# Kernel tuning notes

Hardware: AMD Instinct MI355X
Metric: run time of the kernel (lower is better)

## Reference

```python
import jax, jax.numpy as jnp
import numpy as np

B, S, T = 32, 128, 128
V, E, H = 32000, 256, 256
PAD_IDX = 0


def setup_inputs() -> dict:
    key = jax.random.key(0)
    ks = jax.random.split(key, 12)
    p = lambda k, shape: jax.random.normal(k, shape, dtype=jnp.float32) * 0.05
    src = jax.random.randint(ks[0], (B, S), 0, V)
    tgt = jax.random.randint(ks[1], (B, T), 0, V)
    enc_emb = p(ks[2], (V, E)).at[PAD_IDX].set(0.0)
    dec_emb = p(ks[3], (V, E)).at[PAD_IDX].set(0.0)
    return {
        'src': src,
        'tgt': tgt,
        'enc_emb': enc_emb,
        'enc_Wih': p(ks[4], (4 * H, E)),
        'enc_Whh': p(ks[5], (4 * H, H)),
        'enc_b': p(ks[6], (4 * H,)),
        'dec_emb': dec_emb,
        'dec_Wih': p(ks[7], (4 * H, E)),
        'dec_Whh': p(ks[8], (4 * H, H)),
        'dec_b': p(ks[9], (4 * H,)),
        'fc_W': p(ks[10], (V, H)),
        'fc_b': p(ks[11], (V,)),
    }


def lstm_scan(x_seq, h0, c0, Wih, Whh, b):
    # x_seq: [L, B, E] -> hs: [L, B, H]; PyTorch gate order i, f, g, o
    def step(carry, x):
        h, c = carry
        gates = x @ Wih.T + h @ Whh.T + b  # [B, 4H]
        i, f, g, o = jnp.split(gates, 4, axis=-1)
        c = jax.nn.sigmoid(f) * c + jax.nn.sigmoid(i) * jnp.tanh(g)
        h = jax.nn.sigmoid(o) * jnp.tanh(c)
        return (h, c), h
    (h, c), hs = jax.lax.scan(step, (h0, c0), x_seq)
    return hs, (h, c)


def reference(src, tgt, enc_emb, enc_Wih, enc_Whh, enc_b,
              dec_emb, dec_Wih, dec_Whh, dec_b, fc_W, fc_b):
    bs, tgt_len = tgt.shape
    # Encoder: embed + single-layer LSTM, keep final (h, c)
    x = jnp.swapaxes(enc_emb[src], 0, 1)            # [S, B, E]
    h0 = jnp.zeros((bs, enc_Whh.shape[1]), x.dtype)
    _, (h, c) = lstm_scan(x, h0, h0, enc_Wih, enc_Whh, enc_b)
    # Decoder with full teacher forcing (tf_ratio=1.0):
    # input at step t is tgt[:, t-1]; outputs[:, 0] stays zero.
    dec_in = jnp.swapaxes(dec_emb[tgt[:, :-1]], 0, 1)  # [T-1, B, E]
    hs, _ = lstm_scan(dec_in, h, c, dec_Wih, dec_Whh, dec_b)  # [T-1, B, H]
    logits = jnp.einsum('tbh,vh->btv', hs, fc_W) + fc_b        # [B, T-1, V]
    outputs = jnp.zeros((bs, tgt_len, fc_W.shape[0]), logits.dtype)
    return outputs.at[:, 1:].set(logits)
```

## Files before the change

kernel.cpp:

```cpp
#include <hip/hip_runtime.h>


typedef __attribute__((ext_vector_type(8))) short bf16x8;
typedef __attribute__((ext_vector_type(4))) float f32x4;
typedef __attribute__((ext_vector_type(8))) unsigned short u16x8;
typedef __attribute__((ext_vector_type(4))) unsigned int u32x4;
typedef __attribute__((ext_vector_type(8))) _Float16 f16x8;
typedef __attribute__((ext_vector_type(2))) _Float16 h2;

#define WS_XG_E   0u
#define WS_XG_D   16777216u
#define WS_FCW    33423360u
#define WS_HS     49807360u
#define WS_WTE    51904512u
#define WS_WTD    52428800u

#define KC_REG 48
#define KC_LDS 16

__device__ __forceinline__ unsigned short f2bf(float f) {
  unsigned u = __float_as_uint(f);
  u += 0x7FFFu + ((u >> 16) & 1u);
  return (unsigned short)(u >> 16);
}

__device__ __forceinline__ float sigf(float x) {
  float e = __expf(-x);
  return __builtin_amdgcn_rcpf(1.f + e);
}
__device__ __forceinline__ float tanh_fast(float x) {
  float e = __expf(-2.f * x);
  return fmaf(2.f, __builtin_amdgcn_rcpf(1.f + e), -1.f);
}

#if __has_builtin(__builtin_amdgcn_fdot2)
#define FDOT2(a, w, h) a = __builtin_amdgcn_fdot2(w, h, a, false)
#else
#define FDOT2(a, w, h) a = fmaf((float)w[0], (float)h[0], fmaf((float)w[1], (float)h[1], a))
#endif

__device__ __forceinline__ void dot8(const u16x8 w, const u32x4 hbits,
                                     float& a0, float& a1) {
  f16x8 wv = __builtin_bit_cast(f16x8, w);
  f16x8 hv = __builtin_bit_cast(f16x8, hbits);
  h2 w0 = {wv[0], wv[1]}, w1 = {wv[2], wv[3]};
  h2 w2 = {wv[4], wv[5]}, w3 = {wv[6], wv[7]};
  h2 h0 = {hv[0], hv[1]}, h1 = {hv[2], hv[3]};
  h2 hc = {hv[4], hv[5]}, h3 = {hv[6], hv[7]};
  FDOT2(a0, w0, h0);
  FDOT2(a1, w1, h1);
  FDOT2(a0, w2, hc);
  FDOT2(a1, w3, h3);
}

__global__ __launch_bounds__(256) void zero_col0(float* __restrict__ out) {
  int i = blockIdx.x * 256 + threadIdx.x;
  int b = i / 8000;
  int r = i - b * 8000;
  f32x4 z = {0.f, 0.f, 0.f, 0.f};
  __builtin_nontemporal_store(z, (f32x4*)out + b * 1024000 + r);
}

__global__ __launch_bounds__(256) void cvt_bf16(const float* __restrict__ in,
                                                unsigned short* __restrict__ o,
                                                int n4) {
  int i = blockIdx.x * 256 + threadIdx.x;
  if (i < n4) {
    float4 v = ((const float4*)in)[i];
    ushort4 u;
    u.x = f2bf(v.x); u.y = f2bf(v.y); u.z = f2bf(v.z); u.w = f2bf(v.w);
    *(ushort4*)(o + i * 4) = u;
  }
}

__global__ __launch_bounds__(256) void prep_whalf(const float* __restrict__ We,
                                                  const float* __restrict__ Wd,
                                                  unsigned short* __restrict__ Te,
                                                  unsigned short* __restrict__ Td) {
  int d = blockIdx.x * 256 + threadIdx.x;
  const float* W = blockIdx.y ? Wd : We;
  unsigned short* T = blockIdx.y ? Td : Te;
  int e = d & 7;
  int tmp = d >> 3;
  int tidb = tmp & 511;
  int j = tmp >> 9;
  int gg = j >> 4, kk = j & 15;
  int wv = tidb >> 6, ln = tidb & 63;
  int qq = ln >> 5, dm = wv * 32 + (ln & 31);
  _Float16 v = (_Float16)W[(gg * 256 + dm) * 256 + qq * 128 + kk * 8 + e];
  T[d] = __builtin_bit_cast(unsigned short, v);
}

__global__ __launch_bounds__(256) void xg_gemm(
    const int* __restrict__ tok, const float* __restrict__ emb,
    const float* __restrict__ Wih, const float* __restrict__ bias,
    float* __restrict__ xg, const int Mrows) {
  __shared__ unsigned short As[128][264];
  __shared__ unsigned short Bs[128][264];
  const int tid = threadIdx.x;
  const int nb = blockIdx.x, rb = blockIdx.y;
  {
    int lr = tid >> 1, half = tid & 1;
    int cb = half * 128;
    int row = rb * 128 + lr;
    int rowc = row < Mrows ? row : (Mrows - 1);
    int tt = rowc >> 5, bb = rowc & 31;
    int tk = tok[bb * 128 + tt];
    const float4* sa = (const float4*)(emb + tk * 256 + cb);
    const float4* sb = (const float4*)(Wih + (nb * 128 + lr) * 256 + cb);
#pragma unroll
    for (int i = 0; i < 32; ++i) {
      float4 v = sa[i];
      ushort4 u;
      u.x = f2bf(v.x); u.y = f2bf(v.y); u.z = f2bf(v.z); u.w = f2bf(v.w);
      *(ushort4*)&As[lr][cb + i * 4] = u;
      float4 v2 = sb[i];
      ushort4 u2;
      u2.x = f2bf(v2.x); u2.y = f2bf(v2.y); u2.z = f2bf(v2.z); u2.w = f2bf(v2.w);
      *(ushort4*)&Bs[lr][cb + i * 4] = u2;
    }
  }
  __syncthreads();
  const int lane = tid & 63, w = tid >> 6;
  const int wr = w >> 1, wc = w & 1;
  const int fr = lane & 15, kg = lane >> 4;
  f32x4 acc[4][4];
  const f32x4 zero = {0.f, 0.f, 0.f, 0.f};
#pragma unroll
  for (int mi = 0; mi < 4; ++mi)
#pragma unroll
    for (int ni = 0; ni < 4; ++ni) acc[mi][ni] = zero;
#pragma unroll
  for (int ks = 0; ks < 8; ++ks) {
    const int kb = ks * 32 + kg * 8;
    bf16x8 a[4], b[4];
#pragma unroll
    for (int mi = 0; mi < 4; ++mi)
      a[mi] = *(const bf16x8*)&As[wr * 64 + mi * 16 + fr][kb];
#pragma unroll
    for (int ni = 0; ni < 4; ++ni)
      b[ni] = *(const bf16x8*)&Bs[wc * 64 + ni * 16 + fr][kb];
#pragma unroll
    for (int mi = 0; mi < 4; ++mi)
#pragma unroll
      for (int ni = 0; ni < 4; ++ni)
        acc[mi][ni] = __builtin_amdgcn_mfma_f32_16x16x32_bf16(a[mi], b[ni], acc[mi][ni], 0, 0, 0);
  }
#pragma unroll
  for (int ni = 0; ni < 4; ++ni) {
    const int colg = nb * 128 + wc * 64 + ni * 16 + fr;
    const float bv = bias[colg];
#pragma unroll
    for (int mi = 0; mi < 4; ++mi) {
#pragma unroll
      for (int r = 0; r < 4; ++r) {
        int rowg = rb * 128 + wr * 64 + mi * 16 + kg * 4 + r;
        if (rowg < Mrows) xg[rowg * 1024 + colg] = acc[mi][ni][r] + bv;
      }
    }
  }
}

__global__ __launch_bounds__(512, 2) void lstm_batch(
    const unsigned short* __restrict__ WTe, const unsigned short* __restrict__ WTd,
    const float* __restrict__ xgE, const float* __restrict__ xgD,
    unsigned short* __restrict__ hs) {
  __shared__ __align__(16) unsigned short hh[2][256];
  __shared__ __align__(16) unsigned short wl[KC_LDS * 4096];
  const int tid = threadIdx.x;
  const int b = blockIdx.x;
  const int l = tid & 63, w = tid >> 6;
  const int q = l >> 5;
  const int dim = w * 32 + (l & 31);
  float c = 0.f;
  int cur = 0;
  if (tid < 256) hh[0][tid] = 0;

  for (int phase = 0; phase < 2; ++phase) {
    const unsigned short* WT = phase ? WTd : WTe;
    const float* xg = phase ? xgD : xgE;
    const int steps = phase ? 127 : 128;
    const u16x8* wsrc = (const u16x8*)WT + tid;
    u16x8 wr[KC_REG];
#pragma unroll
    for (int j = 0; j < KC_REG; ++j) wr[j] = wsrc[j * 512];
    __syncthreads();
    {
      u16x8* ld = (u16x8*)wl + tid;
#pragma unroll
      for (int j = 0; j < KC_LDS; ++j) ld[j * 512] = wsrc[(KC_REG + j) * 512];
    }
    __syncthreads();

    for (int t = 0; t < steps; ++t) {
      const float* xr = xg + (t * 32 + b) * 1024 + dim;
      float x0 = xr[0], x1 = xr[256], x2 = xr[512], x3 = xr[768];
      const u32x4* hq = (const u32x4*)&hh[cur][q * 128];
      const u16x8* wlp = (const u16x8*)wl + tid;
      float ai0 = 0.f, ai1 = 0.f, af0 = 0.f, af1 = 0.f;
      float ag0 = 0.f, ag1 = 0.f, ao0 = 0.f, ao1 = 0.f;
#pragma unroll
      for (int kk = 0; kk < 16; ++kk) {
        u32x4 hv = hq[kk];
        dot8(wr[kk],        hv, ai0, ai1);
        dot8(wr[16 + kk],   hv, af0, af1);
        dot8(wr[32 + kk],   hv, ag0, ag1);
        dot8(wlp[kk * 512], hv, ao0, ao1);
      }
      float gi = ai0 + ai1, gf = af0 + af1;
      float gg = ag0 + ag1, go = ao0 + ao1;
      gi += __shfl_xor(gi, 32, 64);
      gf += __shfl_xor(gf, 32, 64);
      gg += __shfl_xor(gg, 32, 64);
      go += __shfl_xor(go, 32, 64);
      gi += x0; gf += x1; gg += x2; go += x3;
      c = sigf(gf) * c + sigf(gi) * tanh_fast(gg);
      float h = sigf(go) * tanh_fast(c);
      if (l < 32) {
        _Float16 hf = (_Float16)h;
        hh[cur ^ 1][dim] = __builtin_bit_cast(unsigned short, hf);
        if (phase) hs[(b * 128 + t) * 256 + dim] = f2bf(h);
      }
      __syncthreads();
      cur ^= 1;
    }
  }
}

__global__ __launch_bounds__(256) void fc_gemm(
    const unsigned short* __restrict__ hsb, const unsigned short* __restrict__ fwb,
    const float* __restrict__ fcb, float* __restrict__ out) {
  __shared__ __align__(16) char smem[69632];
  typedef unsigned short usrow[136];
  usrow* As = (usrow*)smem;
  usrow* Bs = (usrow*)(smem + 34816);
  const int tid = threadIdx.x;
  const int rb = blockIdx.x, nb = blockIdx.y;
  const int lane = tid & 63, w = tid >> 6;
  const int wr = w >> 1, wc = w & 1;
  const int fr = lane & 15, kg = lane >> 4;
  f32x4 acc[4][4];
  const f32x4 zero = {0.f, 0.f, 0.f, 0.f};
#pragma unroll
  for (int mi = 0; mi < 4; ++mi)
#pragma unroll
    for (int ni = 0; ni < 4; ++ni) acc[mi][ni] = zero;

  const int lr = tid >> 1, half = tid & 1;
#pragma unroll
  for (int p = 0; p < 2; ++p) {
    {
      const u16x8* s = (const u16x8*)(hsb + (rb * 128 + lr) * 256 + p * 128 + half * 64);
      const u16x8* s2 = (const u16x8*)(fwb + (nb * 128 + lr) * 256 + p * 128 + half * 64);
      u16x8* d = (u16x8*)&As[lr][half * 64];
      u16x8* d2 = (u16x8*)&Bs[lr][half * 64];
#pragma unroll
      for (int i = 0; i < 8; ++i) { d[i] = s[i]; d2[i] = s2[i]; }
    }
    __syncthreads();
#pragma unroll
    for (int ks = 0; ks < 4; ++ks) {
      const int kb = ks * 32 + kg * 8;
      bf16x8 a[4], b[4];
#pragma unroll
      for (int mi = 0; mi < 4; ++mi)
        a[mi] = *(const bf16x8*)&As[wr * 64 + mi * 16 + fr][kb];
#pragma unroll
      for (int ni = 0; ni < 4; ++ni)
        b[ni] = *(const bf16x8*)&Bs[wc * 64 + ni * 16 + fr][kb];
#pragma unroll
      for (int mi = 0; mi < 4; ++mi)
#pragma unroll
        for (int ni = 0; ni < 4; ++ni)
          acc[mi][ni] = __builtin_amdgcn_mfma_f32_16x16x32_bf16(a[mi], b[ni], acc[mi][ni], 0, 0, 0);
    }
    __syncthreads();
  }
  typedef float frow[132];
  frow* Ct = (frow*)smem;
#pragma unroll
  for (int ni = 0; ni < 4; ++ni) {
    const int cl = wc * 64 + ni * 16 + fr;
    const float bv = fcb[nb * 128 + cl];
#pragma unroll
    for (int mi = 0; mi < 4; ++mi) {
#pragma unroll
      for (int r = 0; r < 4; ++r)
        Ct[wr * 64 + mi * 16 + kg * 4 + r][cl] = acc[mi][ni][r] + bv;
    }
  }
  __syncthreads();
  const int rr = tid >> 5, cc = (tid & 31) * 4;
#pragma unroll
  for (int p = 0; p < 16; ++p) {
    int r = p * 8 + rr;
    if (r != 127) {
      float* dst = out + (size_t)(rb * 128 + r + 1) * 32000 + nb * 128 + cc;
      f32x4 v = *(const f32x4*)&Ct[r][cc];
      __builtin_nontemporal_store(v, (f32x4*)dst);
    }
  }
}

extern "C" void kernel_launch(void* const* d_in, const int* in_sizes, int n_in,
                              void* d_out, int out_size, void* d_ws, size_t ws_size,
                              hipStream_t stream) {
  const int* src = (const int*)d_in[0];
  const int* tgt = (const int*)d_in[1];
  const float* enc_emb = (const float*)d_in[2];
  const float* enc_Wih = (const float*)d_in[3];
  const float* enc_Whh = (const float*)d_in[4];
  const float* enc_b = (const float*)d_in[5];
  const float* dec_emb = (const float*)d_in[6];
  const float* dec_Wih = (const float*)d_in[7];
  const float* dec_Whh = (const float*)d_in[8];
  const float* dec_b = (const float*)d_in[9];
  const float* fc_W = (const float*)d_in[10];
  const float* fc_b = (const float*)d_in[11];
  float* out = (float*)d_out;
  char* ws = (char*)d_ws;

  float* xg_e = (float*)(ws + WS_XG_E);
  float* xg_d = (float*)(ws + WS_XG_D);
  unsigned short* fcw = (unsigned short*)(ws + WS_FCW);
  unsigned short* hs = (unsigned short*)(ws + WS_HS);
  unsigned short* wte = (unsigned short*)(ws + WS_WTE);
  unsigned short* wtd = (unsigned short*)(ws + WS_WTD);

  zero_col0<<<1000, 256, 0, stream>>>(out);
  cvt_bf16<<<8000, 256, 0, stream>>>(fc_W, fcw, 2048000);
  prep_whalf<<<dim3(1024, 2), 256, 0, stream>>>(enc_Whh, dec_Whh, wte, wtd);
  xg_gemm<<<dim3(8, 32), 256, 0, stream>>>(src, enc_emb, enc_Wih, enc_b, xg_e, 4096);
  xg_gemm<<<dim3(8, 32), 256, 0, stream>>>(tgt, dec_emb, dec_Wih, dec_b, xg_d, 4064);
  lstm_batch<<<32, 512, 0, stream>>>(wte, wtd, xg_e, xg_d, hs);
  fc_gemm<<<dim3(32, 250), 256, 0, stream>>>(hs, fcw, fc_b, out);
}
```

Baseline: 678.4 us.

## Halve fc_gemm LDS by reading A fragments from global and staging output in halves

The FC GEMM no longer stages the hidden-state tile in shared memory. Each wave now loads its A fragments straight from global memory, which is small and cache-resident. The output epilogue is split into two 64-row passes so the C staging buffer fits in the same 34 KB, and launch bounds request 4 blocks per CU. Together these cut LDS use in half to allow more resident blocks. The cost is uncoalesced global A loads in the inner loop and an extra barrier round in the epilogue.

```diff
diff --git a/kernel.cpp b/kernel.cpp
--- a/kernel.cpp
+++ b/kernel.cpp
@@ -227,13 +227,12 @@
   }
 }
 
-__global__ __launch_bounds__(256) void fc_gemm(
+__global__ __launch_bounds__(256, 4) void fc_gemm(
     const unsigned short* __restrict__ hsb, const unsigned short* __restrict__ fwb,
     const float* __restrict__ fcb, float* __restrict__ out) {
-  __shared__ __align__(16) char smem[69632];
+  __shared__ __align__(16) char smem[34816];
   typedef unsigned short usrow[136];
-  usrow* As = (usrow*)smem;
-  usrow* Bs = (usrow*)(smem + 34816);
+  usrow* Bs = (usrow*)smem;
   const int tid = threadIdx.x;
   const int rb = blockIdx.x, nb = blockIdx.y;
   const int lane = tid & 63, w = tid >> 6;
@@ -247,15 +246,14 @@
     for (int ni = 0; ni < 4; ++ni) acc[mi][ni] = zero;
 
   const int lr = tid >> 1, half = tid & 1;
+  const unsigned short* arow = hsb + (rb * 128 + wr * 64 + fr) * 256;
 #pragma unroll
   for (int p = 0; p < 2; ++p) {
     {
-      const u16x8* s = (const u16x8*)(hsb + (rb * 128 + lr) * 256 + p * 128 + half * 64);
       const u16x8* s2 = (const u16x8*)(fwb + (nb * 128 + lr) * 256 + p * 128 + half * 64);
-      u16x8* d = (u16x8*)&As[lr][half * 64];
       u16x8* d2 = (u16x8*)&Bs[lr][half * 64];
 #pragma unroll
-      for (int i = 0; i < 8; ++i) { d[i] = s[i]; d2[i] = s2[i]; }
+      for (int i = 0; i < 8; ++i) d2[i] = s2[i];
     }
     __syncthreads();
 #pragma unroll
@@ -264,7 +262,7 @@
       bf16x8 a[4], b[4];
 #pragma unroll
       for (int mi = 0; mi < 4; ++mi)
-        a[mi] = *(const bf16x8*)&As[wr * 64 + mi * 16 + fr][kb];
+        a[mi] = *(const bf16x8*)(arow + mi * 4096 + p * 128 + kb);
 #pragma unroll
       for (int ni = 0; ni < 4; ++ni)
         b[ni] = *(const bf16x8*)&Bs[wc * 64 + ni * 16 + fr][kb];
@@ -276,29 +274,35 @@
     }
     __syncthreads();
   }
+  float bvv[4];
+#pragma unroll
+  for (int ni = 0; ni < 4; ++ni) bvv[ni] = fcb[nb * 128 + wc * 64 + ni * 16 + fr];
   typedef float frow[132];
   frow* Ct = (frow*)smem;
-#pragma unroll
-  for (int ni = 0; ni < 4; ++ni) {
-    const int cl = wc * 64 + ni * 16 + fr;
-    const float bv = fcb[nb * 128 + cl];
-#pragma unroll
-    for (int mi = 0; mi < 4; ++mi) {
-#pragma unroll
-      for (int r = 0; r < 4; ++r)
-        Ct[wr * 64 + mi * 16 + kg * 4 + r][cl] = acc[mi][ni][r] + bv;
-    }
-  }
-  __syncthreads();
   const int rr = tid >> 5, cc = (tid & 31) * 4;
 #pragma unroll
-  for (int p = 0; p < 16; ++p) {
-    int r = p * 8 + rr;
-    if (r != 127) {
-      float* dst = out + (size_t)(rb * 128 + r + 1) * 32000 + nb * 128 + cc;
-      f32x4 v = *(const f32x4*)&Ct[r][cc];
-      __builtin_nontemporal_store(v, (f32x4*)dst);
-    }
+  for (int hh2 = 0; hh2 < 2; ++hh2) {
+    if (wr == hh2) {
+#pragma unroll
+      for (int ni = 0; ni < 4; ++ni)
+#pragma unroll
+        for (int mi = 0; mi < 4; ++mi)
+#pragma unroll
+          for (int r = 0; r < 4; ++r)
+            Ct[mi * 16 + kg * 4 + r][wc * 64 + ni * 16 + fr] = acc[mi][ni][r] + bvv[ni];
+    }
+    __syncthreads();
+#pragma unroll
+    for (int pp = 0; pp < 8; ++pp) {
+      int r = pp * 8 + rr;
+      int tg = hh2 * 64 + r;
+      if (tg != 127) {
+        float* dst = out + (size_t)(rb * 128 + tg + 1) * 32000 + nb * 128 + cc;
+        f32x4 v = *(const f32x4*)&Ct[r][cc];
+        __builtin_nontemporal_store(v, (f32x4*)dst);
+      }
+    }
+    __syncthreads();
   }
 }
 
```

Result: slower. 730.2 us (+7.6%).

## Fuse zero column write into FC GEMM and halve M tile for occupancy

Applied to the files above, without the earlier changes.

Removes the separate zero_col0 kernel and has the FC GEMM write the zero row for t=0 in place of the out-of-range last row. The GEMM M tile shrinks from 128 to 64 rows, which doubles the grid, cuts LDS per block so three blocks can fit per CU, and halves the accumulators per wave. The trade-off is that each weight tile is loaded from global memory twice as often.

```diff
diff --git a/kernel.cpp b/kernel.cpp
--- a/kernel.cpp
+++ b/kernel.cpp
@@ -51,14 +51,6 @@
   FDOT2(a1, w1, h1);
   FDOT2(a0, w2, hc);
   FDOT2(a1, w3, h3);
-}
-
-__global__ __launch_bounds__(256) void zero_col0(float* __restrict__ out) {
-  int i = blockIdx.x * 256 + threadIdx.x;
-  int b = i / 8000;
-  int r = i - b * 8000;
-  f32x4 z = {0.f, 0.f, 0.f, 0.f};
-  __builtin_nontemporal_store(z, (f32x4*)out + b * 1024000 + r);
 }
 
 __global__ __launch_bounds__(256) void cvt_bf16(const float* __restrict__ in,
@@ -227,49 +219,52 @@
   }
 }
 
-__global__ __launch_bounds__(256) void fc_gemm(
+__global__ __launch_bounds__(256, 3) void fc_gemm(
     const unsigned short* __restrict__ hsb, const unsigned short* __restrict__ fwb,
     const float* __restrict__ fcb, float* __restrict__ out) {
-  __shared__ __align__(16) char smem[69632];
+  __shared__ __align__(16) char smem[52224];
   typedef unsigned short usrow[136];
   usrow* As = (usrow*)smem;
-  usrow* Bs = (usrow*)(smem + 34816);
+  usrow* Bs = (usrow*)(smem + 17408);
   const int tid = threadIdx.x;
   const int rb = blockIdx.x, nb = blockIdx.y;
   const int lane = tid & 63, w = tid >> 6;
-  const int wr = w >> 1, wc = w & 1;
+  const int wm = w & 1, wn = w >> 1;
   const int fr = lane & 15, kg = lane >> 4;
-  f32x4 acc[4][4];
+  f32x4 acc[2][4];
   const f32x4 zero = {0.f, 0.f, 0.f, 0.f};
 #pragma unroll
-  for (int mi = 0; mi < 4; ++mi)
+  for (int mi = 0; mi < 2; ++mi)
 #pragma unroll
     for (int ni = 0; ni < 4; ++ni) acc[mi][ni] = zero;
 
-  const int lr = tid >> 1, half = tid & 1;
+  const int ar = tid >> 2, asg = tid & 3;
+  const int br = tid >> 1, bsg = tid & 1;
 #pragma unroll
   for (int p = 0; p < 2; ++p) {
     {
-      const u16x8* s = (const u16x8*)(hsb + (rb * 128 + lr) * 256 + p * 128 + half * 64);
-      const u16x8* s2 = (const u16x8*)(fwb + (nb * 128 + lr) * 256 + p * 128 + half * 64);
-      u16x8* d = (u16x8*)&As[lr][half * 64];
-      u16x8* d2 = (u16x8*)&Bs[lr][half * 64];
-#pragma unroll
-      for (int i = 0; i < 8; ++i) { d[i] = s[i]; d2[i] = s2[i]; }
+      const u16x8* s = (const u16x8*)(hsb + (rb * 64 + ar) * 256 + p * 128 + asg * 32);
+      u16x8* d = (u16x8*)&As[ar][asg * 32];
+#pragma unroll
+      for (int i = 0; i < 4; ++i) d[i] = s[i];
+      const u16x8* s2 = (const u16x8*)(fwb + (nb * 128 + br) * 256 + p * 128 + bsg * 64);
+      u16x8* d2 = (u16x8*)&Bs[br][bsg * 64];
+#pragma unroll
+      for (int i = 0; i < 8; ++i) d2[i] = s2[i];
     }
     __syncthreads();
 #pragma unroll
     for (int ks = 0; ks < 4; ++ks) {
       const int kb = ks * 32 + kg * 8;
-      bf16x8 a[4], b[4];
-#pragma unroll
-      for (int mi = 0; mi < 4; ++mi)
-        a[mi] = *(const bf16x8*)&As[wr * 64 + mi * 16 + fr][kb];
+      bf16x8 a[2], b[4];
+#pragma unroll
+      for (int mi = 0; mi < 2; ++mi)
+        a[mi] = *(const bf16x8*)&As[wm * 32 + mi * 16 + fr][kb];
 #pragma unroll
       for (int ni = 0; ni < 4; ++ni)
-        b[ni] = *(const bf16x8*)&Bs[wc * 64 + ni * 16 + fr][kb];
-#pragma unroll
-      for (int mi = 0; mi < 4; ++mi)
+        b[ni] = *(const bf16x8*)&Bs[wn * 64 + ni * 16 + fr][kb];
+#pragma unroll
+      for (int mi = 0; mi < 2; ++mi)
 #pragma unroll
         for (int ni = 0; ni < 4; ++ni)
           acc[mi][ni] = __builtin_amdgcn_mfma_f32_16x16x32_bf16(a[mi], b[ni], acc[mi][ni], 0, 0, 0);
@@ -280,25 +275,27 @@
   frow* Ct = (frow*)smem;
 #pragma unroll
   for (int ni = 0; ni < 4; ++ni) {
-    const int cl = wc * 64 + ni * 16 + fr;
+    const int cl = wn * 64 + ni * 16 + fr;
     const float bv = fcb[nb * 128 + cl];
 #pragma unroll
-    for (int mi = 0; mi < 4; ++mi) {
+    for (int mi = 0; mi < 2; ++mi) {
 #pragma unroll
       for (int r = 0; r < 4; ++r)
-        Ct[wr * 64 + mi * 16 + kg * 4 + r][cl] = acc[mi][ni][r] + bv;
+        Ct[wm * 32 + mi * 16 + kg * 4 + r][cl] = acc[mi][ni][r] + bv;
     }
   }
   __syncthreads();
+  const int b = rb >> 1, tb = (rb & 1) * 64;
   const int rr = tid >> 5, cc = (tid & 31) * 4;
-#pragma unroll
-  for (int p = 0; p < 16; ++p) {
+  const f32x4 zv = {0.f, 0.f, 0.f, 0.f};
+#pragma unroll
+  for (int p = 0; p < 8; ++p) {
     int r = p * 8 + rr;
-    if (r != 127) {
-      float* dst = out + (size_t)(rb * 128 + r + 1) * 32000 + nb * 128 + cc;
-      f32x4 v = *(const f32x4*)&Ct[r][cc];
-      __builtin_nontemporal_store(v, (f32x4*)dst);
-    }
+    int tg = tb + r;
+    int orow = (tg == 127) ? (b * 128) : (b * 128 + tg + 1);
+    float* dst = out + (size_t)orow * 32000 + nb * 128 + cc;
+    f32x4 v = (tg == 127) ? zv : *(const f32x4*)&Ct[r][cc];
+    __builtin_nontemporal_store(v, (f32x4*)dst);
   }
 }
 
@@ -327,11 +324,10 @@
   unsigned short* wte = (unsigned short*)(ws + WS_WTE);
   unsigned short* wtd = (unsigned short*)(ws + WS_WTD);
 
-  zero_col0<<<1000, 256, 0, stream>>>(out);
   cvt_bf16<<<8000, 256, 0, stream>>>(fc_W, fcw, 2048000);
   prep_whalf<<<dim3(1024, 2), 256, 0, stream>>>(enc_Whh, dec_Whh, wte, wtd);
   xg_gemm<<<dim3(8, 32), 256, 0, stream>>>(src, enc_emb, enc_Wih, enc_b, xg_e, 4096);
   xg_gemm<<<dim3(8, 32), 256, 0, stream>>>(tgt, dec_emb, dec_Wih, dec_b, xg_d, 4064);
   lstm_batch<<<32, 512, 0, stream>>>(wte, wtd, xg_e, xg_d, hs);
-  fc_gemm<<<dim3(32, 250), 256, 0, stream>>>(hs, fcw, fc_b, out);
-}
+  fc_gemm<<<dim3(64, 250), 256, 0, stream>>>(hs, fcw, fc_b, out);
+}
```

Result: faster. 662.3 us (-2.4%).
